# Performance work log

Measured on AMD Instinct MI355X. Metric: run time of the kernel, lower is better.

The kernel has to match this reference:

```python
import jax, jax.numpy as jnp
import numpy as np

N = 1_000_000
D_IN = 128
D_OUT = 64
NUM_CLASSES = 64


def setup_inputs() -> dict:
    key = jax.random.key(0)
    k1, k2, k3, k4 = jax.random.split(key, 4)
    inputs = jax.random.normal(k1, (N, D_IN), dtype=jnp.float32)
    labels = jax.random.randint(k2, (N,), 0, NUM_CLASSES, dtype=jnp.int32)
    # Linear embedding parameters
    W = jax.random.normal(k3, (D_IN, D_OUT), dtype=jnp.float32) / np.sqrt(D_IN)
    b = jax.random.normal(k4, (D_OUT,), dtype=jnp.float32) * 0.01
    return {"inputs": inputs, "labels": labels, "W": W, "b": b}


def reference(inputs, labels, W, b):
    # embedding: simple linear map  [N, D_IN] -> [N, D_OUT]
    emb = jnp.einsum("nd,de->ne", inputs, W) + b
    # per-class mean pooling (prototype): segment sum / segment count
    seg_sum = jax.ops.segment_sum(emb, labels, num_segments=NUM_CLASSES)  # [C, D_OUT]
    counts = jax.ops.segment_sum(jnp.ones((inputs.shape[0],), dtype=emb.dtype),
                                 labels, num_segments=NUM_CLASSES)  # [C]
    protos = seg_sum / jnp.maximum(counts, 1.0)[:, None]
    return protos
```

## Files before the change

kernel.cpp:

```cpp
#include <hip/hip_runtime.h>

#define C_CLASSES 64
#define D_IN 128
#define D_OUT 64


typedef __attribute__((ext_vector_type(8))) __bf16 bf16x8;
typedef __attribute__((ext_vector_type(8))) unsigned short us8;
typedef __attribute__((ext_vector_type(4))) float f32x4;

union frag_cast { us8 u; bf16x8 b; };

__device__ __forceinline__ unsigned short f2bf(float f) {
    unsigned u = __float_as_uint(f);
    unsigned r = u + 0x7FFFu + ((u >> 16) & 1u);
    return (unsigned short)(r >> 16);
}

__global__ __launch_bounds__(256) void seg_mm_kernel(
    const float* __restrict__ x, const int* __restrict__ labels,
    float* __restrict__ gsum, int n)
{
    const int lane  = threadIdx.x & 63;
    const int wave  = threadIdx.x >> 6;
    const int n16   = lane & 15;
    const int quad  = lane >> 4;
    const int cb    = wave * 32;

    f32x4 acc[4][2];
#pragma unroll
    for (int t = 0; t < 4; ++t)
#pragma unroll
        for (int u = 0; u < 2; ++u)
            acc[t][u] = (f32x4){0.f, 0.f, 0.f, 0.f};

    const int stride = (int)gridDim.x * 32;

    for (int rb = (int)blockIdx.x * 32; rb < n; rb += stride) {
        const int4 l0 = *(const int4*)(labels + rb + quad * 8);
        const int4 l1 = *(const int4*)(labels + rb + quad * 8 + 4);
        const int labv[8] = {l0.x, l0.y, l0.z, l0.w, l1.x, l1.y, l1.z, l1.w};

        const float* xp = x + (size_t)(rb + quad * 8) * D_IN + cb + n16;
        float bflt[2][8];
#pragma unroll
        for (int j = 0; j < 8; ++j) {
            bflt[0][j] = xp[(size_t)j * D_IN];
            bflt[1][j] = xp[(size_t)j * D_IN + 16];
        }

        frag_cast bfrag[2];
#pragma unroll
        for (int u = 0; u < 2; ++u)
#pragma unroll
            for (int j = 0; j < 8; ++j)
                bfrag[u].u[j] = f2bf(bflt[u][j]);

        frag_cast afrag[4];
#pragma unroll
        for (int t = 0; t < 4; ++t)
#pragma unroll
            for (int j = 0; j < 8; ++j)
                afrag[t].u[j] = (labv[j] == t * 16 + n16) ? (unsigned short)0x3F80u
                                                          : (unsigned short)0u;

#pragma unroll
        for (int t = 0; t < 4; ++t)
#pragma unroll
            for (int u = 0; u < 2; ++u)
                acc[t][u] = __builtin_amdgcn_mfma_f32_16x16x32_bf16(
                    afrag[t].b, bfrag[u].b, acc[t][u], 0, 0, 0);
    }

#pragma unroll
    for (int t = 0; t < 4; ++t)
#pragma unroll
        for (int u = 0; u < 2; ++u)
#pragma unroll
            for (int r = 0; r < 4; ++r)
                unsafeAtomicAdd(&gsum[(t * 16 + quad * 4 + r) * D_IN + cb + u * 16 + n16],
                                acc[t][u][r]);
}

__global__ __launch_bounds__(256) void count_kernel(
    const int* __restrict__ labels, float* __restrict__ gcnt, int n)
{
    const int lane = threadIdx.x & 63;
    const int gw   = (int)(blockIdx.x * blockDim.x + threadIdx.x) >> 6;
    const int nw   = (int)(gridDim.x * blockDim.x) >> 6;

    int cnt = 0;
    for (int base = gw * 64; base < n; base += nw * 64) {
        const int lab = labels[base + lane];
#pragma unroll
        for (int c = 0; c < C_CLASSES; ++c) {
            unsigned long long m = __ballot(lab == c);
            cnt += (lane == c) ? __popcll(m) : 0;
        }
    }
    unsafeAtomicAdd(&gcnt[lane], (float)cnt);
}

__global__ __launch_bounds__(256) void proto_kernel(
    const float* __restrict__ gsum, const float* __restrict__ gcnt,
    const float* __restrict__ W, const float* __restrict__ b,
    float* __restrict__ out)
{
    const int t = (int)(blockIdx.x * blockDim.x + threadIdx.x);
    const int c = t >> 6;
    const int e = t & 63;

    const float* srow = gsum + (c << 7);
    float acc = 0.0f;
#pragma unroll
    for (int k = 0; k < D_IN; ++k)
        acc = fmaf(srow[k], W[k * D_OUT + e], acc);

    const float cnt = gcnt[c];
    out[(c << 6) + e] = (acc + cnt * b[e]) / fmaxf(cnt, 1.0f);
}

extern "C" void kernel_launch(void* const* d_in, const int* in_sizes, int n_in,
                              void* d_out, int out_size, void* d_ws, size_t ws_size,
                              hipStream_t stream)
{
    const float* x      = (const float*)d_in[0];
    const int*   labels = (const int*)d_in[1];
    const float* W      = (const float*)d_in[2];
    const float* b      = (const float*)d_in[3];
    float*       out    = (float*)d_out;

    float* gsum = (float*)d_ws;
    float* gcnt = gsum + C_CLASSES * D_IN;
    const int n = in_sizes[0] / D_IN;

    hipMemsetAsync(d_ws, 0, (C_CLASSES * D_IN + C_CLASSES) * sizeof(float), stream);

    seg_mm_kernel<<<1024, 256, 0, stream>>>(x, labels, gsum, n);

    count_kernel<<<256, 256, 0, stream>>>(labels, gcnt, n);

    proto_kernel<<<(C_CLASSES * D_OUT) / 256, 256, 0, stream>>>(gsum, gcnt, W, b, out);
}
```

Baseline: 736.8 us.

## Double-buffer input rows into LDS via async global_load_lds prefetch

The segment-matmul kernel now stages each 32-row chunk of the input into shared memory with direct global-to-LDS loads. It prefetches the next chunk and its labels while the current chunk is converted and fed to MFMA, replacing the strided per-thread global loads. This is meant to hide memory latency and coalesce the loads, at the cost of 32 KB of LDS per block, two block barriers per iteration, and possibly lower occupancy.

```diff
diff --git a/kernel.cpp b/kernel.cpp
--- a/kernel.cpp
+++ b/kernel.cpp
@@ -3,6 +3,8 @@
 #define C_CLASSES 64
 #define D_IN 128
 #define D_OUT 64
+#define CHUNK 32
+#define CHUNK_FLTS (CHUNK * D_IN)
 
 
 typedef __attribute__((ext_vector_type(8))) __bf16 bf16x8;
@@ -17,15 +19,23 @@
     return (unsigned short)(r >> 16);
 }
 
+__device__ __forceinline__ void stage16(const float* g, float* l) {
+    __builtin_amdgcn_global_load_lds(
+        (const __attribute__((address_space(1))) unsigned int*)g,
+        (__attribute__((address_space(3))) unsigned int*)l, 16, 0, 0);
+}
+
 __global__ __launch_bounds__(256) void seg_mm_kernel(
     const float* __restrict__ x, const int* __restrict__ labels,
     float* __restrict__ gsum, int n)
 {
-    const int lane  = threadIdx.x & 63;
-    const int wave  = threadIdx.x >> 6;
-    const int n16   = lane & 15;
-    const int quad  = lane >> 4;
-    const int cb    = wave * 32;
+    __shared__ float buf[2][CHUNK_FLTS];
+
+    const int lane = threadIdx.x & 63;
+    const int wave = threadIdx.x >> 6;
+    const int n16  = lane & 15;
+    const int quad = lane >> 4;
+    const int cb   = wave * 32;
 
     f32x4 acc[4][2];
 #pragma unroll
@@ -34,35 +44,54 @@
         for (int u = 0; u < 2; ++u)
             acc[t][u] = (f32x4){0.f, 0.f, 0.f, 0.f};
 
-    const int stride = (int)gridDim.x * 32;
+    const int stride = (int)gridDim.x * CHUNK;
+    const int rb0    = (int)blockIdx.x * CHUNK;
+    const int lslice = wave * 256;
+    const int gslice = lslice + lane * 4;
 
-    for (int rb = (int)blockIdx.x * 32; rb < n; rb += stride) {
-        const int4 l0 = *(const int4*)(labels + rb + quad * 8);
-        const int4 l1 = *(const int4*)(labels + rb + quad * 8 + 4);
-        const int labv[8] = {l0.x, l0.y, l0.z, l0.w, l1.x, l1.y, l1.z, l1.w};
+    if (rb0 < n) {
+#pragma unroll
+        for (int r = 0; r < 4; ++r)
+            stage16(x + (size_t)rb0 * D_IN + r * 1024 + gslice,
+                    &buf[0][r * 1024 + lslice]);
+    }
+    int4 pl0 = {0,0,0,0}, pl1 = {0,0,0,0};
+    if (rb0 < n) {
+        pl0 = *(const int4*)(labels + rb0 + quad * 8);
+        pl1 = *(const int4*)(labels + rb0 + quad * 8 + 4);
+    }
 
-        const float* xp = x + (size_t)(rb + quad * 8) * D_IN + cb + n16;
-        float bflt[2][8];
+    int bufi = 0;
+    for (int rb = rb0; rb < n; rb += stride, bufi ^= 1) {
+        __syncthreads();
+
+        const int rbn = rb + stride;
+        const int labv[8] = {pl0.x, pl0.y, pl0.z, pl0.w,
+                             pl1.x, pl1.y, pl1.z, pl1.w};
+        if (rbn < n) {
 #pragma unroll
-        for (int j = 0; j < 8; ++j) {
-            bflt[0][j] = xp[(size_t)j * D_IN];
-            bflt[1][j] = xp[(size_t)j * D_IN + 16];
+            for (int r = 0; r < 4; ++r)
+                stage16(x + (size_t)rbn * D_IN + r * 1024 + gslice,
+                        &buf[bufi ^ 1][r * 1024 + lslice]);
+            pl0 = *(const int4*)(labels + rbn + quad * 8);
+            pl1 = *(const int4*)(labels + rbn + quad * 8 + 4);
         }
 
+        const float* lb = &buf[bufi][(quad * 8) * D_IN + cb + n16];
         frag_cast bfrag[2];
 #pragma unroll
         for (int u = 0; u < 2; ++u)
 #pragma unroll
             for (int j = 0; j < 8; ++j)
-                bfrag[u].u[j] = f2bf(bflt[u][j]);
+                bfrag[u].u[j] = f2bf(lb[j * D_IN + u * 16]);
 
         frag_cast afrag[4];
 #pragma unroll
         for (int t = 0; t < 4; ++t)
 #pragma unroll
             for (int j = 0; j < 8; ++j)
-                afrag[t].u[j] = (labv[j] == t * 16 + n16) ? (unsigned short)0x3F80u
-                                                          : (unsigned short)0u;
+                afrag[t].u[j] = (labv[j] == t * 16 + n16)
+                                    ? (unsigned short)0x3F80u : (unsigned short)0u;
 
 #pragma unroll
         for (int t = 0; t < 4; ++t)
@@ -70,6 +99,8 @@
             for (int u = 0; u < 2; ++u)
                 acc[t][u] = __builtin_amdgcn_mfma_f32_16x16x32_bf16(
                     afrag[t].b, bfrag[u].b, acc[t][u], 0, 0, 0);
+
+        __syncthreads();
     }
 
 #pragma unroll
```

Result: faster. 707.9 us (-3.9%).
